# Kernel optimization log

Measured on AMD Instinct MI355X. Metric: run time of the kernel, lower is better.

Reference implementation:

```python
import jax, jax.numpy as jnp
import numpy as np

B, D_IN, D_H = 8192, 1024, 1024

def setup_inputs() -> dict:
    key = jax.random.key(0)
    ks = jax.random.split(key, 20)
    s_in = 1.0 / np.sqrt(D_IN)
    s_h = 1.0 / np.sqrt(D_H)
    inp = {
        'input': jax.random.normal(ks[0], (B, D_IN), jnp.float32),
        'h_0': jax.random.normal(ks[1], (B, D_H), jnp.float32),
        'c_0': jax.random.normal(ks[2], (B, D_H), jnp.float32),
    }
    names = ['i', 'f', 'g', 'o']
    for idx, g in enumerate(names):
        inp[f'W_{g}_i2h'] = jax.random.uniform(ks[3 + 4 * idx], (D_H, D_IN), jnp.float32, -s_in, s_in)
        inp[f'b_{g}_i2h'] = jax.random.uniform(ks[4 + 4 * idx], (D_H,), jnp.float32, -s_in, s_in)
        inp[f'W_{g}_h2h'] = jax.random.uniform(ks[5 + 4 * idx], (D_H, D_H), jnp.float32, -s_h, s_h)
        inp[f'b_{g}_h2h'] = jax.random.uniform(ks[6 + 4 * idx], (D_H,), jnp.float32, -s_h, s_h)
    return inp


def reference(input, h_0, c_0,
              W_i_i2h, b_i_i2h, W_i_h2h, b_i_h2h,
              W_f_i2h, b_f_i2h, W_f_h2h, b_f_h2h,
              W_g_i2h, b_g_i2h, W_g_h2h, b_g_h2h,
              W_o_i2h, b_o_i2h, W_o_h2h, b_o_h2h):
    # pre-activations: x @ W_i2h^T + b + h @ W_h2h^T + b  (Linear uses y = x W^T + b)
    def lin(x, W, b):
        return x @ W.T + b
    it = jax.nn.sigmoid(lin(input, W_i_i2h, b_i_i2h) + lin(h_0, W_i_h2h, b_i_h2h))
    ft = jax.nn.sigmoid(lin(input, W_f_i2h, b_f_i2h) + lin(h_0, W_f_h2h, b_f_h2h))
    ot = jax.nn.sigmoid(lin(input, W_o_i2h, b_o_i2h) + lin(h_0, W_o_h2h, b_o_h2h))
    gt = jnp.tanh(lin(input, W_g_i2h, b_g_i2h) + lin(h_0, W_g_h2h, b_g_h2h))
    ct = ft * c_0 + it * gt
    output = ot * jnp.tanh(ct)
    return (output, ct)
```

## Files before the change

kernel.cpp:

```cpp
#include <hip/hip_runtime.h>
#include <cstdint>

typedef __attribute__((ext_vector_type(8))) short bf16x8;
typedef __attribute__((ext_vector_type(4))) float f32x4;
typedef __attribute__((ext_vector_type(8))) unsigned short u16x8;

typedef __attribute__((address_space(1))) unsigned int gu32_t;
typedef __attribute__((address_space(3))) unsigned int lu32_t;

#define BATCH 8192
#define DIN 1024
#define DH 1024
#define KD 2048
#define ND 4096

__device__ __forceinline__ unsigned short f2bf(float f) {
    union { float f; unsigned int u; } v; v.f = f;
    unsigned int u = v.u;
    u += 0x7fffu + ((u >> 16) & 1u);
    return (unsigned short)(u >> 16);
}
__device__ __forceinline__ float sigmoidf_(float x) {
    return 1.0f / (1.0f + __expf(-x));
}
__device__ __forceinline__ float tanhf_(float x) {
    float xc = fminf(fmaxf(x, -15.0f), 15.0f);
    float e2 = __expf(2.0f * xc);
    return (e2 - 1.0f) / (e2 + 1.0f);
}
__device__ __forceinline__ int fswz(int r) {
    return ((r & 3) << 4) ^ ((r & 4) << 3);
}

__global__ void __launch_bounds__(256) convert_all(
        const float* __restrict__ x, const float* __restrict__ h,
        const float* __restrict__ Wii, const float* __restrict__ Wih,
        const float* __restrict__ Wfi, const float* __restrict__ Wfh,
        const float* __restrict__ Wgi, const float* __restrict__ Wgh,
        const float* __restrict__ Woi, const float* __restrict__ Woh,
        const float* __restrict__ bii, const float* __restrict__ bih,
        const float* __restrict__ bfi, const float* __restrict__ bfh,
        const float* __restrict__ bgi, const float* __restrict__ bgh,
        const float* __restrict__ boi, const float* __restrict__ boh,
        unsigned short* __restrict__ A, unsigned short* __restrict__ B,
        float* __restrict__ bsum) {
    const int t = blockIdx.x * 256 + threadIdx.x;
    if (t < 2097152) {
        const int64_t off = (int64_t)t * 8;
        const int row = (int)(off >> 11);
        const int k = (int)(off & 2047);
        const float* src = (k < DIN) ? (x + (int64_t)row * DIN + k)
                                     : (h + (int64_t)row * DH + (k - DIN));
        f32x4 v0 = *(const f32x4*)src;
        f32x4 v1 = *(const f32x4*)(src + 4);
        u16x8 o;
        o[0] = f2bf(v0[0]); o[1] = f2bf(v0[1]); o[2] = f2bf(v0[2]); o[3] = f2bf(v0[3]);
        o[4] = f2bf(v1[0]); o[5] = f2bf(v1[1]); o[6] = f2bf(v1[2]); o[7] = f2bf(v1[3]);
        *(u16x8*)(A + off) = o;
    } else if (t < 3145728) {
        const int tb = t - 2097152;
        const int64_t off = (int64_t)tb * 8;
        const int brow = (int)(off >> 11);
        const int k = (int)(off & 2047);
        const int gate = brow & 3;
        const int n = brow >> 2;
        const float* Wi2h = (gate == 0) ? Wii : (gate == 1) ? Wfi : (gate == 2) ? Wgi : Woi;
        const float* Wh2h = (gate == 0) ? Wih : (gate == 1) ? Wfh : (gate == 2) ? Wgh : Woh;
        const float* src = (k < 1024) ? (Wi2h + (int64_t)n * 1024 + k)
                                      : (Wh2h + (int64_t)n * 1024 + (k - 1024));
        f32x4 v0 = *(const f32x4*)src;
        f32x4 v1 = *(const f32x4*)(src + 4);
        u16x8 o;
        o[0] = f2bf(v0[0]); o[1] = f2bf(v0[1]); o[2] = f2bf(v0[2]); o[3] = f2bf(v0[3]);
        o[4] = f2bf(v1[0]); o[5] = f2bf(v1[1]); o[6] = f2bf(v1[2]); o[7] = f2bf(v1[3]);
        *(u16x8*)(B + off) = o;
    } else {
        const int b = t - 3145728;
#pragma unroll
        for (int i = 0; i < 8; ++i) {
            const int e = b * 8 + i;
            const int n = e >> 2;
            const int g = e & 3;
            const float* bi = (g == 0) ? bii : (g == 1) ? bfi : (g == 2) ? bgi : boi;
            const float* bh = (g == 0) ? bih : (g == 1) ? bfh : (g == 2) ? bgh : boh;
            bsum[e] = bi[n] + bh[n];
        }
    }
}

__global__ void __launch_bounds__(512, 2) gemm_lstm(
        const unsigned short* __restrict__ A,
        const unsigned short* __restrict__ Bw,
        const float* __restrict__ c0p,
        const float* __restrict__ bsum,
        float* __restrict__ outp) {
    __shared__ __align__(16) unsigned short lds[4][16384];

    const int bid = blockIdx.x;
    const int swz = ((bid & 7) << 6) | (bid >> 3);
    const int bm = swz & 31;
    const int bn = swz >> 5;
    const int t = threadIdx.x;
    const int lane = t & 63;
    const int wave = t >> 6;
    const int wm = wave >> 2;
    const int wn = wave & 3;

    f32x4 acc[8][4];
#pragma unroll
    for (int m = 0; m < 8; ++m)
#pragma unroll
        for (int n = 0; n < 4; ++n)
            acc[m][n] = (f32x4){0.f, 0.f, 0.f, 0.f};

    const int crow = t >> 2;
    const int kb = ((t & 3) << 4) ^ fswz(crow & 7);
    const unsigned short* aS0 = A  + (size_t)(bm * 256 + crow) * KD + (kb >> 1);
    const unsigned short* aS1 = aS0 + (size_t)128 * KD;
    const unsigned short* bS0 = Bw + (size_t)(bn * 256 + crow) * KD + (kb >> 1);
    const unsigned short* bS1 = bS0 + (size_t)128 * KD;
    const int ldsDst = wave * 512;

    const int r15 = lane & 15;
    const int rdk = ((((lane >> 4) << 4) ^ fswz(r15 & 7)) >> 1);
    const int aoff = r15 * 32 + rdk;
    const int aRowBase = (wm * 128) * 32;
    const int bRowBase = 8192 + (wn * 64) * 32;

#pragma unroll
    for (int pt = 0; pt < 3; ++pt) {
        unsigned short* dA = &lds[pt][ldsDst];
        unsigned short* dB = &lds[pt][8192 + ldsDst];
        __builtin_amdgcn_global_load_lds((const gu32_t*)(aS0 + pt * 32), (lu32_t*)dA, 16, 0, 0);
        __builtin_amdgcn_global_load_lds((const gu32_t*)(aS1 + pt * 32), (lu32_t*)(dA + 4096), 16, 0, 0);
        __builtin_amdgcn_global_load_lds((const gu32_t*)(bS0 + pt * 32), (lu32_t*)dB, 16, 0, 0);
        __builtin_amdgcn_global_load_lds((const gu32_t*)(bS1 + pt * 32), (lu32_t*)(dB + 4096), 16, 0, 0);
    }
    asm volatile("s_waitcnt vmcnt(8)" ::: "memory");
    __builtin_amdgcn_sched_barrier(0);
    __builtin_amdgcn_s_barrier();
    __builtin_amdgcn_sched_barrier(0);

    for (int tt = 0; tt < 16; ++tt) {
#pragma unroll
        for (int q = 0; q < 4; ++q) {
            const int t64 = tt * 4 + q;
            if (t64 < 61) {
                const int b3 = (q + 3) & 3;
                unsigned short* dA = &lds[b3][ldsDst];
                unsigned short* dB = &lds[b3][8192 + ldsDst];
                const size_t ko = (size_t)(t64 + 3) * 32;
                __builtin_amdgcn_global_load_lds((const gu32_t*)(aS0 + ko), (lu32_t*)dA, 16, 0, 0);
                __builtin_amdgcn_global_load_lds((const gu32_t*)(aS1 + ko), (lu32_t*)(dA + 4096), 16, 0, 0);
                __builtin_amdgcn_global_load_lds((const gu32_t*)(bS0 + ko), (lu32_t*)dB, 16, 0, 0);
                __builtin_amdgcn_global_load_lds((const gu32_t*)(bS1 + ko), (lu32_t*)(dB + 4096), 16, 0, 0);
            }
            const unsigned short* aB = &lds[q][aRowBase + aoff];
            const unsigned short* bB = &lds[q][bRowBase + aoff];
            bf16x8 af[8], bf4[4];
#pragma unroll
            for (int m = 0; m < 8; ++m) af[m] = *(const bf16x8*)(aB + m * 512);
#pragma unroll
            for (int n = 0; n < 4; ++n) bf4[n] = *(const bf16x8*)(bB + n * 512);
            __builtin_amdgcn_s_setprio(1);
#pragma unroll
            for (int m = 0; m < 8; ++m)
#pragma unroll
                for (int n = 0; n < 4; ++n)
                    acc[m][n] = __builtin_amdgcn_mfma_f32_16x16x32_bf16(af[m], bf4[n], acc[m][n], 0, 0, 0);
            __builtin_amdgcn_s_setprio(0);
            if (t64 < 61)       asm volatile("s_waitcnt vmcnt(8)" ::: "memory");
            else if (t64 == 61) asm volatile("s_waitcnt vmcnt(4)" ::: "memory");
            else if (t64 == 62) asm volatile("s_waitcnt vmcnt(0)" ::: "memory");
            if (t64 < 63) {
                __builtin_amdgcn_sched_barrier(0);
                __builtin_amdgcn_s_barrier();
                __builtin_amdgcn_sched_barrier(0);
            }
        }
    }

    float* pre = (float*)&lds[0][0];
    const int lr = t >> 3;
    const int cg = t & 7;
    const int rswz = (lr & 7) << 2;
#pragma unroll
    for (int c = 0; c < 4; ++c) {
        __syncthreads();
        if (wm == (c >> 1)) {
#pragma unroll
            for (int mm = 0; mm < 4; ++mm) {
                const int m = (c & 1) * 4 + mm;
#pragma unroll
                for (int n = 0; n < 4; ++n) {
                    const int col = wn * 64 + n * 16 + r15;
#pragma unroll
                    for (int j = 0; j < 4; ++j) {
                        const int rw = mm * 16 + ((lane >> 4) << 2) + j;
                        pre[rw * 256 + (col ^ ((rw & 7) << 2))] = acc[m][n][j];
                    }
                }
            }
        }
        __syncthreads();
        const int R = bm * 256 + c * 64 + lr;
        const int64_t eo = (int64_t)R * DH + bn * 64 + cg * 8;
        f32x4 cp0 = *(const f32x4*)&c0p[eo];
        f32x4 cp1 = *(const f32x4*)&c0p[eo + 4];
        float hbuf[8], cbuf[8];
#pragma unroll
        for (int g8 = 0; g8 < 8; ++g8) {
            const int colf = cg * 32 + g8 * 4;
            f32x4 pr = *(const f32x4*)&pre[lr * 256 + (colf ^ rswz)];
            f32x4 bs = *(const f32x4*)&bsum[bn * 256 + colf];
            float it = sigmoidf_(pr[0] + bs[0]);
            float ft = sigmoidf_(pr[1] + bs[1]);
            float gt = tanhf_(pr[2] + bs[2]);
            float ot = sigmoidf_(pr[3] + bs[3]);
            float cprev = (g8 < 4) ? cp0[g8 & 3] : cp1[g8 & 3];
            float ct = ft * cprev + it * gt;
            cbuf[g8] = ct;
            hbuf[g8] = ot * tanhf_(ct);
        }
        f32x4 h0v = {hbuf[0], hbuf[1], hbuf[2], hbuf[3]};
        f32x4 h1v = {hbuf[4], hbuf[5], hbuf[6], hbuf[7]};
        f32x4 c0v = {cbuf[0], cbuf[1], cbuf[2], cbuf[3]};
        f32x4 c1v = {cbuf[4], cbuf[5], cbuf[6], cbuf[7]};
        *(f32x4*)&outp[eo] = h0v;
        *(f32x4*)&outp[eo + 4] = h1v;
        *(f32x4*)&outp[(int64_t)BATCH * DH + eo] = c0v;
        *(f32x4*)&outp[(int64_t)BATCH * DH + eo + 4] = c1v;
    }
}

extern "C" void kernel_launch(void* const* d_in, const int* in_sizes, int n_in,
                              void* d_out, int out_size, void* d_ws, size_t ws_size,
                              hipStream_t stream) {
    const float* x   = (const float*)d_in[0];
    const float* h0  = (const float*)d_in[1];
    const float* c0  = (const float*)d_in[2];
    const float* Wii = (const float*)d_in[3];
    const float* bii = (const float*)d_in[4];
    const float* Wih = (const float*)d_in[5];
    const float* bih = (const float*)d_in[6];
    const float* Wfi = (const float*)d_in[7];
    const float* bfi = (const float*)d_in[8];
    const float* Wfh = (const float*)d_in[9];
    const float* bfh = (const float*)d_in[10];
    const float* Wgi = (const float*)d_in[11];
    const float* bgi = (const float*)d_in[12];
    const float* Wgh = (const float*)d_in[13];
    const float* bgh = (const float*)d_in[14];
    const float* Woi = (const float*)d_in[15];
    const float* boi = (const float*)d_in[16];
    const float* Woh = (const float*)d_in[17];
    const float* boh = (const float*)d_in[18];

    unsigned short* A  = (unsigned short*)d_ws;
    unsigned short* Bw = A + (size_t)BATCH * KD;
    float* bsum = (float*)(Bw + (size_t)ND * KD);
    float* out = (float*)d_out;

    convert_all<<<12290, 256, 0, stream>>>(x, h0,
        Wii, Wih, Wfi, Wfh, Wgi, Wgh, Woi, Woh,
        bii, bih, bfi, bfh, bgi, bgh, boi, boh,
        A, Bw, bsum);
    gemm_lstm<<<512, 512, 0, stream>>>(A, Bw, c0, bsum, out);
}
```

Before: 334.2 us.

## Restructure GEMM main loop into K=64 double-buffered tiles with split-quadrant staging

Replaces the 4-stage K=32 ring buffer with a 2-buffer K=64 scheme. Each wave now computes four quadrant sub-blocks (two M halves by two N halves), and async global-to-LDS loads for the next tile are interleaved between quadrant MFMA phases. The LDS layout and swizzle change to 8-slot XOR rows, and the epilogue is remapped to the new accumulator layout. The aim is to halve the K iterations and overlap loads with MFMA at finer grain, at the cost of more barriers per tile and more delicate waitcnt accounting.

```diff
diff --git a/kernel.cpp b/kernel.cpp
--- a/kernel.cpp
+++ b/kernel.cpp
@@ -27,9 +27,6 @@
     float xc = fminf(fmaxf(x, -15.0f), 15.0f);
     float e2 = __expf(2.0f * xc);
     return (e2 - 1.0f) / (e2 + 1.0f);
-}
-__device__ __forceinline__ int fswz(int r) {
-    return ((r & 3) << 4) ^ ((r & 4) << 3);
 }
 
 __global__ void __launch_bounds__(256) convert_all(
@@ -88,13 +85,17 @@
     }
 }
 
+#define SB  __builtin_amdgcn_sched_barrier(0)
+#define BAR __builtin_amdgcn_s_barrier()
+#define LGKM0 asm volatile("s_waitcnt lgkmcnt(0)" ::: "memory")
+
 __global__ void __launch_bounds__(512, 2) gemm_lstm(
         const unsigned short* __restrict__ A,
         const unsigned short* __restrict__ Bw,
         const float* __restrict__ c0p,
         const float* __restrict__ bsum,
         float* __restrict__ outp) {
-    __shared__ __align__(16) unsigned short lds[4][16384];
+    __shared__ __align__(16) unsigned short lds[65536];
 
     const int bid = blockIdx.x;
     const int swz = ((bid & 7) << 6) | (bid >> 3);
@@ -106,101 +107,126 @@
     const int wm = wave >> 2;
     const int wn = wave & 3;
 
-    f32x4 acc[8][4];
-#pragma unroll
-    for (int m = 0; m < 8; ++m)
-#pragma unroll
-        for (int n = 0; n < 4; ++n)
-            acc[m][n] = (f32x4){0.f, 0.f, 0.f, 0.f};
-
-    const int crow = t >> 2;
-    const int kb = ((t & 3) << 4) ^ fswz(crow & 7);
-    const unsigned short* aS0 = A  + (size_t)(bm * 256 + crow) * KD + (kb >> 1);
-    const unsigned short* aS1 = aS0 + (size_t)128 * KD;
-    const unsigned short* bS0 = Bw + (size_t)(bn * 256 + crow) * KD + (kb >> 1);
-    const unsigned short* bS1 = bS0 + (size_t)128 * KD;
-    const int ldsDst = wave * 512;
+    f32x4 acc[2][2][4][2];
+#pragma unroll
+    for (int a = 0; a < 2; ++a)
+#pragma unroll
+        for (int b = 0; b < 2; ++b)
+#pragma unroll
+            for (int m = 0; m < 4; ++m)
+#pragma unroll
+                for (int n = 0; n < 2; ++n)
+                    acc[a][b][m][n] = (f32x4){0.f, 0.f, 0.f, 0.f};
+
+    const int srow = t >> 3;
+    const int sslot = (t & 7) ^ (srow & 7);
+    const unsigned short* aSrc = A  + (size_t)(bm * 256 + srow) * KD + sslot * 8;
+    const unsigned short* bSrc = Bw + (size_t)(bn * 256 + srow) * KD + sslot * 8;
+    const int dstOff = wave * 512;
+
+#define STAGE_A(D, H, KT) do { \
+    const unsigned short* _s = aSrc + (size_t)(H) * 128 * KD + (size_t)(KT) * 64; \
+    __builtin_amdgcn_global_load_lds((const gu32_t*)_s, (lu32_t*)&lds[(D)*16384 + (H)*8192 + dstOff], 16, 0, 0); \
+    __builtin_amdgcn_global_load_lds((const gu32_t*)(_s + (size_t)64 * KD), (lu32_t*)&lds[(D)*16384 + (H)*8192 + dstOff + 4096], 16, 0, 0); \
+  } while (0)
+#define STAGE_B(D, H, KT) do { \
+    const unsigned short* _s = bSrc + (size_t)(H) * 128 * KD + (size_t)(KT) * 64; \
+    __builtin_amdgcn_global_load_lds((const gu32_t*)_s, (lu32_t*)&lds[32768 + (D)*16384 + (H)*8192 + dstOff], 16, 0, 0); \
+    __builtin_amdgcn_global_load_lds((const gu32_t*)(_s + (size_t)64 * KD), (lu32_t*)&lds[32768 + (D)*16384 + (H)*8192 + dstOff + 4096], 16, 0, 0); \
+  } while (0)
 
     const int r15 = lane & 15;
-    const int rdk = ((((lane >> 4) << 4) ^ fswz(r15 & 7)) >> 1);
-    const int aoff = r15 * 32 + rdk;
-    const int aRowBase = (wm * 128) * 32;
-    const int bRowBase = 8192 + (wn * 64) * 32;
-
-#pragma unroll
-    for (int pt = 0; pt < 3; ++pt) {
-        unsigned short* dA = &lds[pt][ldsDst];
-        unsigned short* dB = &lds[pt][8192 + ldsDst];
-        __builtin_amdgcn_global_load_lds((const gu32_t*)(aS0 + pt * 32), (lu32_t*)dA, 16, 0, 0);
-        __builtin_amdgcn_global_load_lds((const gu32_t*)(aS1 + pt * 32), (lu32_t*)(dA + 4096), 16, 0, 0);
-        __builtin_amdgcn_global_load_lds((const gu32_t*)(bS0 + pt * 32), (lu32_t*)dB, 16, 0, 0);
-        __builtin_amdgcn_global_load_lds((const gu32_t*)(bS1 + pt * 32), (lu32_t*)(dB + 4096), 16, 0, 0);
+    const int g4 = lane >> 4;
+    const int x7 = r15 & 7;
+    const int slotE0 = (g4 ^ x7) * 8;
+    const int slotE1 = ((4 | g4) ^ x7) * 8;
+    const int aRowOff = (wm * 64 + r15) * 64;
+    const int bRowOff = 32768 + (wn * 32 + r15) * 64;
+
+#define LDA(D, MH, M, SL) (*(const bf16x8*)&lds[(D)*16384 + (MH)*8192 + aRowOff + (M)*1024 + (SL)])
+#define LDB(D, NH, N, SL) (*(const bf16x8*)&lds[(D)*16384 + (NH)*8192 + bRowOff + (N)*1024 + (SL)])
+
+    bf16x8 af[2][4], bf[2][2][2];
+
+#define MFMA_Q(MH, NH) do { \
+    __builtin_amdgcn_s_setprio(1); \
+    _Pragma("unroll") \
+    for (int kk = 0; kk < 2; ++kk) \
+      _Pragma("unroll") \
+      for (int m = 0; m < 4; ++m) \
+        _Pragma("unroll") \
+        for (int n = 0; n < 2; ++n) \
+          acc[MH][NH][m][n] = __builtin_amdgcn_mfma_f32_16x16x32_bf16(af[kk][m], bf[NH][kk][n], acc[MH][NH][m][n], 0, 0, 0); \
+    __builtin_amdgcn_s_setprio(0); \
+  } while (0)
+
+#define KTILE(D, T64) do { \
+    const int dn_ = (D) ^ 1; \
+     \
+    _Pragma("unroll") for (int m = 0; m < 4; ++m) af[0][m] = LDA(D, 0, m, slotE0); \
+    _Pragma("unroll") for (int m = 0; m < 4; ++m) af[1][m] = LDA(D, 0, m, slotE1); \
+    _Pragma("unroll") for (int n = 0; n < 2; ++n) bf[0][0][n] = LDB(D, 0, n, slotE0); \
+    _Pragma("unroll") for (int n = 0; n < 2; ++n) bf[0][1][n] = LDB(D, 0, n, slotE1); \
+    if ((T64) < 31) STAGE_A(dn_, 1, (T64) + 1); \
+    SB; BAR; LGKM0; SB; \
+    MFMA_Q(0, 0); \
+    if ((T64) == 31) asm volatile("s_waitcnt vmcnt(0)" ::: "memory"); \
+    SB; BAR; \
+     \
+    _Pragma("unroll") for (int n = 0; n < 2; ++n) bf[1][0][n] = LDB(D, 1, n, slotE0); \
+    _Pragma("unroll") for (int n = 0; n < 2; ++n) bf[1][1][n] = LDB(D, 1, n, slotE1); \
+    if ((T64) < 31) STAGE_B(dn_, 1, (T64) + 1); \
+    SB; BAR; LGKM0; SB; \
+    MFMA_Q(0, 1); \
+    SB; BAR; \
+     \
+    _Pragma("unroll") for (int m = 0; m < 4; ++m) af[0][m] = LDA(D, 1, m, slotE0); \
+    _Pragma("unroll") for (int m = 0; m < 4; ++m) af[1][m] = LDA(D, 1, m, slotE1); \
+    if ((T64) < 30) STAGE_A(D, 0, (T64) + 2); \
+    SB; BAR; LGKM0; SB; \
+    MFMA_Q(1, 0); \
+    SB; BAR; \
+     \
+    if ((T64) < 30) STAGE_B(D, 0, (T64) + 2); \
+    SB; BAR; SB; \
+    MFMA_Q(1, 1); \
+    if ((T64) < 31) asm volatile("s_waitcnt vmcnt(4)" ::: "memory"); \
+    SB; BAR; \
+  } while (0)
+
+    STAGE_A(0, 0, 0); STAGE_B(0, 0, 0); STAGE_A(0, 1, 0); STAGE_B(0, 1, 0);
+    STAGE_A(1, 0, 1); STAGE_B(1, 0, 1);
+    asm volatile("s_waitcnt vmcnt(4)" ::: "memory");
+    SB; BAR; SB;
+
+    for (int tp = 0; tp < 16; ++tp) {
+        const int t0 = tp * 2;
+        KTILE(0, t0);
+        KTILE(1, t0 + 1);
     }
-    asm volatile("s_waitcnt vmcnt(8)" ::: "memory");
-    __builtin_amdgcn_sched_barrier(0);
-    __builtin_amdgcn_s_barrier();
-    __builtin_amdgcn_sched_barrier(0);
-
-    for (int tt = 0; tt < 16; ++tt) {
-#pragma unroll
-        for (int q = 0; q < 4; ++q) {
-            const int t64 = tt * 4 + q;
-            if (t64 < 61) {
-                const int b3 = (q + 3) & 3;
-                unsigned short* dA = &lds[b3][ldsDst];
-                unsigned short* dB = &lds[b3][8192 + ldsDst];
-                const size_t ko = (size_t)(t64 + 3) * 32;
-                __builtin_amdgcn_global_load_lds((const gu32_t*)(aS0 + ko), (lu32_t*)dA, 16, 0, 0);
-                __builtin_amdgcn_global_load_lds((const gu32_t*)(aS1 + ko), (lu32_t*)(dA + 4096), 16, 0, 0);
-                __builtin_amdgcn_global_load_lds((const gu32_t*)(bS0 + ko), (lu32_t*)dB, 16, 0, 0);
-                __builtin_amdgcn_global_load_lds((const gu32_t*)(bS1 + ko), (lu32_t*)(dB + 4096), 16, 0, 0);
-            }
-            const unsigned short* aB = &lds[q][aRowBase + aoff];
-            const unsigned short* bB = &lds[q][bRowBase + aoff];
-            bf16x8 af[8], bf4[4];
-#pragma unroll
-            for (int m = 0; m < 8; ++m) af[m] = *(const bf16x8*)(aB + m * 512);
-#pragma unroll
-            for (int n = 0; n < 4; ++n) bf4[n] = *(const bf16x8*)(bB + n * 512);
-            __builtin_amdgcn_s_setprio(1);
-#pragma unroll
-            for (int m = 0; m < 8; ++m)
-#pragma unroll
-                for (int n = 0; n < 4; ++n)
-                    acc[m][n] = __builtin_amdgcn_mfma_f32_16x16x32_bf16(af[m], bf4[n], acc[m][n], 0, 0, 0);
-            __builtin_amdgcn_s_setprio(0);
-            if (t64 < 61)       asm volatile("s_waitcnt vmcnt(8)" ::: "memory");
-            else if (t64 == 61) asm volatile("s_waitcnt vmcnt(4)" ::: "memory");
-            else if (t64 == 62) asm volatile("s_waitcnt vmcnt(0)" ::: "memory");
-            if (t64 < 63) {
-                __builtin_amdgcn_sched_barrier(0);
-                __builtin_amdgcn_s_barrier();
-                __builtin_amdgcn_sched_barrier(0);
-            }
-        }
-    }
-
-    float* pre = (float*)&lds[0][0];
+
+    float* pre = (float*)&lds[0];
     const int lr = t >> 3;
     const int cg = t & 7;
     const int rswz = (lr & 7) << 2;
 #pragma unroll
     for (int c = 0; c < 4; ++c) {
         __syncthreads();
-        if (wm == (c >> 1)) {
-#pragma unroll
-            for (int mm = 0; mm < 4; ++mm) {
-                const int m = (c & 1) * 4 + mm;
-#pragma unroll
-                for (int n = 0; n < 4; ++n) {
-                    const int col = wn * 64 + n * 16 + r15;
-#pragma unroll
-                    for (int j = 0; j < 4; ++j) {
-                        const int rw = mm * 16 + ((lane >> 4) << 2) + j;
-                        pre[rw * 256 + (col ^ ((rw & 7) << 2))] = acc[m][n][j];
-                    }
+        if (wm == (c & 1)) {
+            const int mh = c >> 1;
+#pragma unroll
+            for (int nh = 0; nh < 2; ++nh)
+#pragma unroll
+                for (int n = 0; n < 2; ++n) {
+                    const int col = nh * 128 + wn * 32 + n * 16 + r15;
+#pragma unroll
+                    for (int m = 0; m < 4; ++m)
+#pragma unroll
+                        for (int j = 0; j < 4; ++j) {
+                            const int rw = m * 16 + g4 * 4 + j;
+                            pre[rw * 256 + (col ^ ((rw & 7) << 2))] = acc[mh][nh][m][n][j];
+                        }
                 }
-            }
         }
         __syncthreads();
         const int R = bm * 256 + c * 64 + lr;
```

New measurement: 327.7 us. No clear change (-1.9%).
